# Kernel tuning notes

Hardware: AMD Instinct MI355X
Metric: run time of the kernel (lower is better)

## Reference

```python
import jax, jax.numpy as jnp
import numpy as np

N_NODES = 100000


def _sage_conv(x, edge_index, W_n, W_s, b):
    # edge_index: [2, E] with row0 = src, row1 = dst (messages flow src -> dst)
    src, dst = edge_index[0], edge_index[1]
    msgs = x[src]                                   # [E, F] gather
    summed = jax.ops.segment_sum(msgs, dst, num_segments=N_NODES)   # [N, F]
    deg = jax.ops.segment_sum(jnp.ones((edge_index.shape[1],), x.dtype), dst,
                              num_segments=N_NODES)                 # [N]
    mean = summed / jnp.maximum(deg, 1.0)[:, None]  # mean aggregation
    return mean @ W_n + x @ W_s + b


def setup_inputs() -> dict:
    key = jax.random.key(0)
    ks = jax.random.split(key, 8)
    in_dim, hid_dim, out_dim = 64, 64, 32
    n_edges = 1600000
    x = jax.random.normal(ks[0], (N_NODES, in_dim), dtype=jnp.float32)
    edge_index = jax.random.randint(ks[1], (2, n_edges), 0, N_NODES, dtype=jnp.int64)
    s1 = 1.0 / np.sqrt(in_dim)
    s2 = 1.0 / np.sqrt(hid_dim)
    W1_n = jax.random.uniform(ks[2], (in_dim, hid_dim), jnp.float32, -s1, s1)
    W1_s = jax.random.uniform(ks[3], (in_dim, hid_dim), jnp.float32, -s1, s1)
    b1 = jnp.zeros((hid_dim,), jnp.float32)
    W2_n = jax.random.uniform(ks[4], (hid_dim, out_dim), jnp.float32, -s2, s2)
    W2_s = jax.random.uniform(ks[5], (hid_dim, out_dim), jnp.float32, -s2, s2)
    b2 = jnp.zeros((out_dim,), jnp.float32)
    return {"x": x, "edge_index": edge_index, "W1_n": W1_n, "W1_s": W1_s,
            "b1": b1, "W2_n": W2_n, "W2_s": W2_s, "b2": b2}


def reference(x, edge_index, W1_n, W1_s, b1, W2_n, W2_s, b2):
    h = _sage_conv(x, edge_index, W1_n, W1_s, b1)
    h = jax.nn.relu(h)
    # dropout(p=0.5) is identity in eval mode
    out = _sage_conv(h, edge_index, W2_n, W2_s, b2)
    return out
```

## Files before the change

### kernel.cpp

```cpp
#include <hip/hip_runtime.h>
#include <hip/hip_bf16.h>

#define N_NODES 100000
#define NB 784
#define NPAD 100352
#define BSH 7
#define BMASK 127
#define CAP 4096
#define MSTRIDE 36

typedef float v2f __attribute__((ext_vector_type(2)));

__device__ inline void fma4(float a, const float4& w, float4& c) {
  c.x = fmaf(a, w.x, c.x);
  c.y = fmaf(a, w.y, c.y);
  c.z = fmaf(a, w.z, c.z);
  c.w = fmaf(a, w.w, c.w);
}
__device__ inline unsigned short f2bf(float f) {
  unsigned u = __float_as_uint(f);
  u += 0x7fffu + ((u >> 16) & 1u);
  return (unsigned short)(u >> 16);
}
__device__ inline unsigned pack2bf(float a, float b) {
  return (unsigned)f2bf(a) | ((unsigned)f2bf(b) << 16);
}
__device__ inline unsigned packfp8x4(float a, float b, float c, float d) {
  int pk = __builtin_amdgcn_cvt_pk_fp8_f32(a, b, 0, false);
  pk = __builtin_amdgcn_cvt_pk_fp8_f32(c, d, pk, true);
  return (unsigned)pk;
}
__device__ inline float4 relu_mix(uint2 m, uint2 s) {
  float4 v;
  v.x = fmaxf(__uint_as_float(m.x << 16) + __uint_as_float(s.x << 16), 0.f);
  v.y = fmaxf(__uint_as_float(m.x & 0xffff0000u) +
                  __uint_as_float(s.x & 0xffff0000u), 0.f);
  v.z = fmaxf(__uint_as_float(m.y << 16) + __uint_as_float(s.y << 16), 0.f);
  v.w = fmaxf(__uint_as_float(m.y & 0xffff0000u) +
                  __uint_as_float(s.y & 0xffff0000u), 0.f);
  return v;
}

#define EPB 8192
#define EPT 32
#define GB1 1563

__global__ __launch_bounds__(256) void fusedA_k(
    const int* __restrict__ src, const int* __restrict__ dst,
    unsigned* __restrict__ bcur, unsigned* __restrict__ ep,
    const float* __restrict__ x, const float* __restrict__ W1n,
    const float* __restrict__ W1s, const float* __restrict__ b1,
    unsigned* __restrict__ xnb8, unsigned short* __restrict__ xsb,
    int E, int NSB, int M) {
  __shared__ __align__(16) float smem[8192];
  const int tid = threadIdx.x;

  if ((int)blockIdx.x < NSB) {
    unsigned* lh = (unsigned*)smem;
    unsigned* lbase = lh + NB;
    for (int i = tid; i < NB; i += 256) lh[i] = 0;
    __syncthreads();
    const int ebase = blockIdx.x * EPB;
    unsigned rb[EPT];
#pragma unroll
    for (int it = 0; it < EPT; ++it) {
      int e = ebase + it * 256 + tid;
      if (e < E) {
        unsigned b = ((unsigned)dst[e]) >> BSH;
        unsigned r = atomicAdd(&lh[b], 1u);
        rb[it] = (r << 10) | b;
      }
    }
    __syncthreads();
    for (int i = tid; i < NB; i += 256)
      lbase[i] = lh[i] ? atomicAdd(&bcur[i], lh[i]) : 0u;
    __syncthreads();
#pragma unroll
    for (int it = 0; it < EPT; ++it) {
      int e = ebase + it * 256 + tid;
      if (e < E) {
        unsigned b = rb[it] & 1023u;
        unsigned r = rb[it] >> 10;
        ep[(size_t)b * CAP + lbase[b] + r] =
            (((unsigned)src[e]) << BSH) | (((unsigned)dst[e]) & BMASK);
      }
    }
    return;
  }

  float* Wn = smem;
  float* Ws = smem + 4096;
  const int row0 = ((int)blockIdx.x - NSB) * 64;

  for (int i = tid; i < 1024; i += 256) {
    ((float4*)Wn)[i] = ((const float4*)W1n)[i];
    ((float4*)Ws)[i] = ((const float4*)W1s)[i];
  }

  const int tx = tid & 15;
  const int ty = tid >> 4;
  const int arow = ty * 4;

  const float* xr[4];
#pragma unroll
  for (int r = 0; r < 4; ++r) {
    long long gr = row0 + arow + r;
    if (gr >= M) gr = M - 1;
    xr[r] = x + gr * 64;
  }

  float4 an[4], as[4];
#pragma unroll
  for (int r = 0; r < 4; ++r) {
    an[r] = make_float4(0.f, 0.f, 0.f, 0.f);
    as[r] = make_float4(0.f, 0.f, 0.f, 0.f);
  }
  __syncthreads();

#pragma unroll 2
  for (int k4 = 0; k4 < 16; ++k4) {
    float4 a[4];
#pragma unroll
    for (int r = 0; r < 4; ++r) a[r] = *(const float4*)(xr[r] + 4 * k4);
    float4 wn0 = *(const float4*)&Wn[(4 * k4 + 0) * 64 + 4 * tx];
    float4 wn1 = *(const float4*)&Wn[(4 * k4 + 1) * 64 + 4 * tx];
    float4 wn2 = *(const float4*)&Wn[(4 * k4 + 2) * 64 + 4 * tx];
    float4 wn3 = *(const float4*)&Wn[(4 * k4 + 3) * 64 + 4 * tx];
    float4 ws0 = *(const float4*)&Ws[(4 * k4 + 0) * 64 + 4 * tx];
    float4 ws1 = *(const float4*)&Ws[(4 * k4 + 1) * 64 + 4 * tx];
    float4 ws2 = *(const float4*)&Ws[(4 * k4 + 2) * 64 + 4 * tx];
    float4 ws3 = *(const float4*)&Ws[(4 * k4 + 3) * 64 + 4 * tx];
#pragma unroll
    for (int r = 0; r < 4; ++r) {
      fma4(a[r].x, wn0, an[r]);
      fma4(a[r].y, wn1, an[r]);
      fma4(a[r].z, wn2, an[r]);
      fma4(a[r].w, wn3, an[r]);
      fma4(a[r].x, ws0, as[r]);
      fma4(a[r].y, ws1, as[r]);
      fma4(a[r].z, ws2, as[r]);
      fma4(a[r].w, ws3, as[r]);
    }
  }

  const float4 bv = *(const float4*)&b1[4 * tx];
#pragma unroll
  for (int r = 0; r < 4; ++r) {
    int row = row0 + arow + r;
    if (row < M) {
      ushort4 ps;
      ps.x = f2bf(as[r].x + bv.x);
      ps.y = f2bf(as[r].y + bv.y);
      ps.z = f2bf(as[r].z + bv.z);
      ps.w = f2bf(as[r].w + bv.w);
      *(ushort4*)&xsb[(long long)row * 64 + 4 * tx] = ps;
      xnb8[(size_t)row * 16 + tx] =
          packfp8x4(an[r].x, an[r].y, an[r].z, an[r].w);
    }
  }
}

__global__ __launch_bounds__(256) void bsort_k(const unsigned* __restrict__ ep,
                                               const unsigned* __restrict__ bcur,
                                               int* __restrict__ ssrc,
                                               uint2* __restrict__ rows2) {
  __shared__ unsigned cnt[128];
  __shared__ unsigned sc[128];
  const int tid = threadIdx.x;
  const int b = blockIdx.x;
  const unsigned cntb = bcur[b];
  const unsigned beg = (unsigned)(b * CAP);
  if (tid < 128) cnt[tid] = 0;
  __syncthreads();
  for (unsigned j = tid; j < cntb; j += 256)
    atomicAdd(&cnt[ep[(size_t)beg + j] & BMASK], 1u);
  __syncthreads();
  unsigned v = (tid < 128) ? cnt[tid] : 0u;
  if (tid < 128) sc[tid] = v;
  __syncthreads();
  for (int off = 1; off < 128; off <<= 1) {
    unsigned t = (tid < 128 && tid >= off) ? sc[tid - off] : 0u;
    __syncthreads();
    if (tid < 128) sc[tid] += t;
    __syncthreads();
  }
  if (tid < 128) {
    unsigned ex = sc[tid] - v;
    rows2[b * 128 + tid] = make_uint2(beg + ex, beg + ex + v);
    cnt[tid] = ex;
  }
  __syncthreads();
  for (unsigned j = tid; j < cntb; j += 256) {
    unsigned p = ep[(size_t)beg + j];
    unsigned r = atomicAdd(&cnt[p & BMASK], 1u);
    ssrc[(size_t)beg + r] = (int)(p >> BSH);
  }
}

__global__ __launch_bounds__(256) void fgg_k(
    const uint4* __restrict__ valb4, const int* __restrict__ ssrc,
    const uint2* __restrict__ rows2, const unsigned short* __restrict__ xsb,
    const float* __restrict__ W2n, const float* __restrict__ W2s,
    const float* __restrict__ b2, unsigned* __restrict__ hnb8,
    float* __restrict__ hs, int M) {
  __shared__ float Wn[64 * 32];
  __shared__ float Ws[64 * 32];
  __shared__ unsigned mlds[64 * MSTRIDE];
  const int tid = threadIdx.x;
  const int node0 = blockIdx.x * 64;

  for (int i = tid; i < 512; i += 256) {
    ((float4*)Wn)[i] = ((const float4*)W2n)[i];
    ((float4*)Ws)[i] = ((const float4*)W2s)[i];
  }

  constexpr int P = 4;
  const int lrow = tid / P;
  const int node = node0 + lrow;
  const int p = tid & 3;
  const uint2 be = rows2[node];
  const unsigned beg = be.x, end = be.y;

  float acc[16];
#pragma unroll
  for (int q = 0; q < 16; ++q) acc[q] = 0.f;

  unsigned j = beg;
  for (; j + 8 <= end; j += 8) {
    int sn[8];
#pragma unroll
    for (int i = 0; i < 8; ++i) sn[i] = ssrc[j + i];
    uint4 u[8];
#pragma unroll
    for (int i = 0; i < 8; ++i) u[i] = valb4[(size_t)sn[i] * P + p];
#pragma unroll
    for (int i = 0; i < 8; ++i) {
      v2f f0 = __builtin_amdgcn_cvt_pk_f32_fp8((int)u[i].x, false);
      v2f f1 = __builtin_amdgcn_cvt_pk_f32_fp8((int)u[i].x, true);
      v2f f2 = __builtin_amdgcn_cvt_pk_f32_fp8((int)u[i].y, false);
      v2f f3 = __builtin_amdgcn_cvt_pk_f32_fp8((int)u[i].y, true);
      v2f f4 = __builtin_amdgcn_cvt_pk_f32_fp8((int)u[i].z, false);
      v2f f5 = __builtin_amdgcn_cvt_pk_f32_fp8((int)u[i].z, true);
      v2f f6 = __builtin_amdgcn_cvt_pk_f32_fp8((int)u[i].w, false);
      v2f f7 = __builtin_amdgcn_cvt_pk_f32_fp8((int)u[i].w, true);
      acc[0] += f0[0];  acc[1] += f0[1];
      acc[2] += f1[0];  acc[3] += f1[1];
      acc[4] += f2[0];  acc[5] += f2[1];
      acc[6] += f3[0];  acc[7] += f3[1];
      acc[8] += f4[0];  acc[9] += f4[1];
      acc[10] += f5[0]; acc[11] += f5[1];
      acc[12] += f6[0]; acc[13] += f6[1];
      acc[14] += f7[0]; acc[15] += f7[1];
    }
  }
  if (j < end) {
    const unsigned last = end - 1;
    int sn[8];
#pragma unroll
    for (int i = 0; i < 8; ++i) {
      unsigned jj = j + i;
      sn[i] = ssrc[jj < last ? jj : last];
    }
    uint4 u[8];
#pragma unroll
    for (int i = 0; i < 8; ++i) u[i] = valb4[(size_t)sn[i] * P + p];
#pragma unroll
    for (int i = 0; i < 8; ++i) {
      float w = ((j + i) < end) ? 1.f : 0.f;
      v2f f0 = __builtin_amdgcn_cvt_pk_f32_fp8((int)u[i].x, false);
      v2f f1 = __builtin_amdgcn_cvt_pk_f32_fp8((int)u[i].x, true);
      v2f f2 = __builtin_amdgcn_cvt_pk_f32_fp8((int)u[i].y, false);
      v2f f3 = __builtin_amdgcn_cvt_pk_f32_fp8((int)u[i].y, true);
      v2f f4 = __builtin_amdgcn_cvt_pk_f32_fp8((int)u[i].z, false);
      v2f f5 = __builtin_amdgcn_cvt_pk_f32_fp8((int)u[i].z, true);
      v2f f6 = __builtin_amdgcn_cvt_pk_f32_fp8((int)u[i].w, false);
      v2f f7 = __builtin_amdgcn_cvt_pk_f32_fp8((int)u[i].w, true);
      acc[0] = fmaf(w, f0[0], acc[0]);   acc[1] = fmaf(w, f0[1], acc[1]);
      acc[2] = fmaf(w, f1[0], acc[2]);   acc[3] = fmaf(w, f1[1], acc[3]);
      acc[4] = fmaf(w, f2[0], acc[4]);   acc[5] = fmaf(w, f2[1], acc[5]);
      acc[6] = fmaf(w, f3[0], acc[6]);   acc[7] = fmaf(w, f3[1], acc[7]);
      acc[8] = fmaf(w, f4[0], acc[8]);   acc[9] = fmaf(w, f4[1], acc[9]);
      acc[10] = fmaf(w, f5[0], acc[10]); acc[11] = fmaf(w, f5[1], acc[11]);
      acc[12] = fmaf(w, f6[0], acc[12]); acc[13] = fmaf(w, f6[1], acc[13]);
      acc[14] = fmaf(w, f7[0], acc[14]); acc[15] = fmaf(w, f7[1], acc[15]);
    }
  }

  const unsigned dg = end - beg;
  const float inv = dg ? 1.f / (float)dg : 0.f;
  uint4 pk0, pk1;
  pk0.x = pack2bf(acc[0] * inv, acc[1] * inv);
  pk0.y = pack2bf(acc[2] * inv, acc[3] * inv);
  pk0.z = pack2bf(acc[4] * inv, acc[5] * inv);
  pk0.w = pack2bf(acc[6] * inv, acc[7] * inv);
  pk1.x = pack2bf(acc[8] * inv, acc[9] * inv);
  pk1.y = pack2bf(acc[10] * inv, acc[11] * inv);
  pk1.z = pack2bf(acc[12] * inv, acc[13] * inv);
  pk1.w = pack2bf(acc[14] * inv, acc[15] * inv);
  *(uint4*)&mlds[lrow * MSTRIDE + p * 8] = pk0;
  *(uint4*)&mlds[lrow * MSTRIDE + p * 8 + 4] = pk1;
  __syncthreads();

  const int tx = tid & 7;
  const int ty = tid >> 3;
  const int arow = ty * 2;

  const uint2* mp[2];
  const uint2* sp[2];
#pragma unroll
  for (int r = 0; r < 2; ++r) {
    long long gr = node0 + arow + r;
    if (gr >= M) gr = M - 1;
    mp[r] = (const uint2*)&mlds[(arow + r) * MSTRIDE];
    sp[r] = (const uint2*)(xsb + gr * 64);
  }

  float4 an[2], as[2];
#pragma unroll
  for (int r = 0; r < 2; ++r) {
    an[r] = make_float4(0.f, 0.f, 0.f, 0.f);
    as[r] = make_float4(0.f, 0.f, 0.f, 0.f);
  }

#pragma unroll 2
  for (int k4 = 0; k4 < 16; ++k4) {
    float4 a[2];
#pragma unroll
    for (int r = 0; r < 2; ++r) a[r] = relu_mix(mp[r][k4], sp[r][k4]);
    float4 wn0 = *(const float4*)&Wn[(4 * k4 + 0) * 32 + 4 * tx];
    float4 wn1 = *(const float4*)&Wn[(4 * k4 + 1) * 32 + 4 * tx];
    float4 wn2 = *(const float4*)&Wn[(4 * k4 + 2) * 32 + 4 * tx];
    float4 wn3 = *(const float4*)&Wn[(4 * k4 + 3) * 32 + 4 * tx];
    float4 ws0 = *(const float4*)&Ws[(4 * k4 + 0) * 32 + 4 * tx];
    float4 ws1 = *(const float4*)&Ws[(4 * k4 + 1) * 32 + 4 * tx];
    float4 ws2 = *(const float4*)&Ws[(4 * k4 + 2) * 32 + 4 * tx];
    float4 ws3 = *(const float4*)&Ws[(4 * k4 + 3) * 32 + 4 * tx];
#pragma unroll
    for (int r = 0; r < 2; ++r) {
      fma4(a[r].x, wn0, an[r]);
      fma4(a[r].y, wn1, an[r]);
      fma4(a[r].z, wn2, an[r]);
      fma4(a[r].w, wn3, an[r]);
      fma4(a[r].x, ws0, as[r]);
      fma4(a[r].y, ws1, as[r]);
      fma4(a[r].z, ws2, as[r]);
      fma4(a[r].w, ws3, as[r]);
    }
  }

  const float4 bv = *(const float4*)&b2[4 * tx];
#pragma unroll
  for (int r = 0; r < 2; ++r) {
    int row = node0 + arow + r;
    if (row < M) {
      float4 o;
      o.x = as[r].x + bv.x;
      o.y = as[r].y + bv.y;
      o.z = as[r].z + bv.z;
      o.w = as[r].w + bv.w;
      *(float4*)&hs[(long long)row * 32 + 4 * tx] = o;
      hnb8[(size_t)row * 8 + tx] =
          packfp8x4(an[r].x, an[r].y, an[r].z, an[r].w);
    }
  }
}

__global__ __launch_bounds__(256) void gather2_k(
    const uint4* __restrict__ valb4, const int* __restrict__ ssrc,
    const uint2* __restrict__ rows2, const float* __restrict__ base,
    float* __restrict__ out, int N) {
  constexpr int P = 2;
  const int node = blockIdx.x * 128 + threadIdx.x / P;
  const int p = threadIdx.x & 1;
  if (node >= N) return;
  const uint2 be = rows2[node];
  const unsigned beg = be.x, end = be.y;

  float acc[16];
#pragma unroll
  for (int q = 0; q < 16; ++q) acc[q] = 0.f;

  unsigned j = beg;
  for (; j + 8 <= end; j += 8) {
    int sn[8];
#pragma unroll
    for (int i = 0; i < 8; ++i) sn[i] = ssrc[j + i];
    uint4 u[8];
#pragma unroll
    for (int i = 0; i < 8; ++i) u[i] = valb4[(size_t)sn[i] * P + p];
#pragma unroll
    for (int i = 0; i < 8; ++i) {
      v2f f0 = __builtin_amdgcn_cvt_pk_f32_fp8((int)u[i].x, false);
      v2f f1 = __builtin_amdgcn_cvt_pk_f32_fp8((int)u[i].x, true);
      v2f f2 = __builtin_amdgcn_cvt_pk_f32_fp8((int)u[i].y, false);
      v2f f3 = __builtin_amdgcn_cvt_pk_f32_fp8((int)u[i].y, true);
      v2f f4 = __builtin_amdgcn_cvt_pk_f32_fp8((int)u[i].z, false);
      v2f f5 = __builtin_amdgcn_cvt_pk_f32_fp8((int)u[i].z, true);
      v2f f6 = __builtin_amdgcn_cvt_pk_f32_fp8((int)u[i].w, false);
      v2f f7 = __builtin_amdgcn_cvt_pk_f32_fp8((int)u[i].w, true);
      acc[0] += f0[0];  acc[1] += f0[1];
      acc[2] += f1[0];  acc[3] += f1[1];
      acc[4] += f2[0];  acc[5] += f2[1];
      acc[6] += f3[0];  acc[7] += f3[1];
      acc[8] += f4[0];  acc[9] += f4[1];
      acc[10] += f5[0]; acc[11] += f5[1];
      acc[12] += f6[0]; acc[13] += f6[1];
      acc[14] += f7[0]; acc[15] += f7[1];
    }
  }
  if (j < end) {
    const unsigned last = end - 1;
    int sn[8];
#pragma unroll
    for (int i = 0; i < 8; ++i) {
      unsigned jj = j + i;
      sn[i] = ssrc[jj < last ? jj : last];
    }
    uint4 u[8];
#pragma unroll
    for (int i = 0; i < 8; ++i) u[i] = valb4[(size_t)sn[i] * P + p];
#pragma unroll
    for (int i = 0; i < 8; ++i) {
      float w = ((j + i) < end) ? 1.f : 0.f;
      v2f f0 = __builtin_amdgcn_cvt_pk_f32_fp8((int)u[i].x, false);
      v2f f1 = __builtin_amdgcn_cvt_pk_f32_fp8((int)u[i].x, true);
      v2f f2 = __builtin_amdgcn_cvt_pk_f32_fp8((int)u[i].y, false);
      v2f f3 = __builtin_amdgcn_cvt_pk_f32_fp8((int)u[i].y, true);
      v2f f4 = __builtin_amdgcn_cvt_pk_f32_fp8((int)u[i].z, false);
      v2f f5 = __builtin_amdgcn_cvt_pk_f32_fp8((int)u[i].z, true);
      v2f f6 = __builtin_amdgcn_cvt_pk_f32_fp8((int)u[i].w, false);
      v2f f7 = __builtin_amdgcn_cvt_pk_f32_fp8((int)u[i].w, true);
      acc[0] = fmaf(w, f0[0], acc[0]);   acc[1] = fmaf(w, f0[1], acc[1]);
      acc[2] = fmaf(w, f1[0], acc[2]);   acc[3] = fmaf(w, f1[1], acc[3]);
      acc[4] = fmaf(w, f2[0], acc[4]);   acc[5] = fmaf(w, f2[1], acc[5]);
      acc[6] = fmaf(w, f3[0], acc[6]);   acc[7] = fmaf(w, f3[1], acc[7]);
      acc[8] = fmaf(w, f4[0], acc[8]);   acc[9] = fmaf(w, f4[1], acc[9]);
      acc[10] = fmaf(w, f5[0], acc[10]); acc[11] = fmaf(w, f5[1], acc[11]);
      acc[12] = fmaf(w, f6[0], acc[12]); acc[13] = fmaf(w, f6[1], acc[13]);
      acc[14] = fmaf(w, f7[0], acc[14]); acc[15] = fmaf(w, f7[1], acc[15]);
    }
  }

  const unsigned dg = end - beg;
  const float inv = dg ? 1.f / (float)dg : 0.f;
  const size_t o = (size_t)node * 32 + 16 * p;
#pragma unroll
  for (int q4 = 0; q4 < 4; ++q4) {
    float4 bv = *(const float4*)&base[o + 4 * q4];
    float4 ov;
    ov.x = acc[4 * q4 + 0] * inv + bv.x;
    ov.y = acc[4 * q4 + 1] * inv + bv.y;
    ov.z = acc[4 * q4 + 2] * inv + bv.z;
    ov.w = acc[4 * q4 + 3] * inv + bv.w;
    *(float4*)&out[o + 4 * q4] = ov;
  }
}

extern "C" void kernel_launch(void* const* d_in, const int* in_sizes, int n_in,
                              void* d_out, int out_size, void* d_ws,
                              size_t ws_size, hipStream_t stream) {
  const float* x   = (const float*)d_in[0];
  const int*   ei  = (const int*)d_in[1];
  const float* W1n = (const float*)d_in[2];
  const float* W1s = (const float*)d_in[3];
  const float* b1  = (const float*)d_in[4];
  const float* W2n = (const float*)d_in[5];
  const float* W2s = (const float*)d_in[6];
  const float* b2  = (const float*)d_in[7];
  float* out = (float*)d_out;

  const int E = in_sizes[1] / 2;
  const int M = N_NODES;
  const int* src = ei;
  const int* dst = ei + E;
  const int NSB = (E + EPB - 1) / EPB;

  char* wsb = (char*)d_ws;
  unsigned*       ep    = (unsigned*)(wsb);
  int*            ssrc  = (int*)(wsb + 12845056);
  uint2*          rows2 = (uint2*)(wsb + 25690112);
  unsigned*       bcur  = (unsigned*)(wsb + 26492928);
  unsigned*       xnb8  = (unsigned*)(wsb + 26496064);
  unsigned short* xsb   = (unsigned short*)(wsb + 32896064);
  float*          hs    = (float*)(wsb + 45696064);
  unsigned*       hnb8  = (unsigned*)(wsb);

  hipMemsetAsync(bcur, 0, NB * 4, stream);
  fusedA_k<<<NSB + GB1, 256, 0, stream>>>(src, dst, bcur, ep, x, W1n, W1s, b1,
                                          xnb8, xsb, E, NSB, M);
  bsort_k<<<NB, 256, 0, stream>>>(ep, bcur, ssrc, rows2);
  fgg_k<<<GB1, 256, 0, stream>>>((const uint4*)xnb8, ssrc, rows2, xsb, W2n,
                                 W2s, b2, hnb8, hs, M);
  gather2_k<<<(M + 127) / 128, 256, 0, stream>>>((const uint4*)hnb8, ssrc,
                                                 rows2, hs, out, M);
}
```

Measured before the change: 195.9 us.

## Merge edge binning into GEMM blocks using direct global atomics

Removes the separate edge-binning blocks. Every layer-1 GEMM block now also bins 1024 edges: it loads src/dst, then claims a slot in its destination bucket with one global atomicAdd per edge before starting the GEMM. This drops the shared-memory histogram, its barriers and the extra blocks, and lets edge loads overlap the weight staging. The cost is about 1.6M global atomics on only 784 counters instead of one atomic per bucket per block, which risks heavy contention.

Result: slower. 543.4 us (+177.4%).

```diff
diff --git a/kernel.cpp b/kernel.cpp
--- a/kernel.cpp
+++ b/kernel.cpp
@@ -41,62 +41,51 @@
   return v;
 }
 
-#define EPB 8192
-#define EPT 32
 #define GB1 1563
-
-__global__ __launch_bounds__(256) void fusedA_k(
+#define SEPB 1024
+
+__global__ __launch_bounds__(256) void fusedB_k(
     const int* __restrict__ src, const int* __restrict__ dst,
     unsigned* __restrict__ bcur, unsigned* __restrict__ ep,
     const float* __restrict__ x, const float* __restrict__ W1n,
     const float* __restrict__ W1s, const float* __restrict__ b1,
     unsigned* __restrict__ xnb8, unsigned short* __restrict__ xsb,
-    int E, int NSB, int M) {
+    int E, int M) {
   __shared__ __align__(16) float smem[8192];
-  const int tid = threadIdx.x;
-
-  if ((int)blockIdx.x < NSB) {
-    unsigned* lh = (unsigned*)smem;
-    unsigned* lbase = lh + NB;
-    for (int i = tid; i < NB; i += 256) lh[i] = 0;
-    __syncthreads();
-    const int ebase = blockIdx.x * EPB;
-    unsigned rb[EPT];
-#pragma unroll
-    for (int it = 0; it < EPT; ++it) {
-      int e = ebase + it * 256 + tid;
-      if (e < E) {
-        unsigned b = ((unsigned)dst[e]) >> BSH;
-        unsigned r = atomicAdd(&lh[b], 1u);
-        rb[it] = (r << 10) | b;
-      }
-    }
-    __syncthreads();
-    for (int i = tid; i < NB; i += 256)
-      lbase[i] = lh[i] ? atomicAdd(&bcur[i], lh[i]) : 0u;
-    __syncthreads();
-#pragma unroll
-    for (int it = 0; it < EPT; ++it) {
-      int e = ebase + it * 256 + tid;
-      if (e < E) {
-        unsigned b = rb[it] & 1023u;
-        unsigned r = rb[it] >> 10;
-        ep[(size_t)b * CAP + lbase[b] + r] =
-            (((unsigned)src[e]) << BSH) | (((unsigned)dst[e]) & BMASK);
-      }
-    }
-    return;
-  }
-
   float* Wn = smem;
   float* Ws = smem + 4096;
-  const int row0 = ((int)blockIdx.x - NSB) * 64;
+  const int tid = threadIdx.x;
+  const int bid = blockIdx.x;
+
+  const int ebase = bid * SEPB;
+  int es[4], ed[4];
+  bool ev[4];
+#pragma unroll
+  for (int it = 0; it < 4; ++it) {
+    int e = ebase + it * 256 + tid;
+    ev[it] = (e < E);
+    if (ev[it]) {
+      es[it] = src[e];
+      ed[it] = dst[e];
+    }
+  }
 
   for (int i = tid; i < 1024; i += 256) {
     ((float4*)Wn)[i] = ((const float4*)W1n)[i];
     ((float4*)Ws)[i] = ((const float4*)W1s)[i];
   }
 
+#pragma unroll
+  for (int it = 0; it < 4; ++it) {
+    if (ev[it]) {
+      unsigned b = ((unsigned)ed[it]) >> BSH;
+      unsigned r = atomicAdd(&bcur[b], 1u);
+      ep[(size_t)b * CAP + r] =
+          (((unsigned)es[it]) << BSH) | (((unsigned)ed[it]) & BMASK);
+    }
+  }
+
+  const int row0 = bid * 64;
   const int tx = tid & 15;
   const int ty = tid >> 4;
   const int arow = ty * 4;
@@ -473,7 +462,6 @@
   const int M = N_NODES;
   const int* src = ei;
   const int* dst = ei + E;
-  const int NSB = (E + EPB - 1) / EPB;
 
   char* wsb = (char*)d_ws;
   unsigned*       ep    = (unsigned*)(wsb);
@@ -486,8 +474,8 @@
   unsigned*       hnb8  = (unsigned*)(wsb);
 
   hipMemsetAsync(bcur, 0, NB * 4, stream);
-  fusedA_k<<<NSB + GB1, 256, 0, stream>>>(src, dst, bcur, ep, x, W1n, W1s, b1,
-                                          xnb8, xsb, E, NSB, M);
+  fusedB_k<<<GB1, 256, 0, stream>>>(src, dst, bcur, ep, x, W1n, W1s, b1,
+                                    xnb8, xsb, E, M);
   bsort_k<<<NB, 256, 0, stream>>>(ep, bcur, ssrc, rows2);
   fgg_k<<<GB1, 256, 0, stream>>>((const uint4*)xnb8, ssrc, rows2, xsb, W2n,
                                  W2s, b2, hnb8, hs, M);
```

## Sort nodes by degree within each block to balance gather work per wavefront

Applied to the files above, without the earlier changes.

Both gather kernels now load per-node degrees into shared memory, rank the nodes in the block by degree, and assign threads to nodes in sorted order. Nodes with similar degree then share a wavefront, which is meant to reduce divergence and idle lanes in the edge loop. The tail handling also changes from clamped-index loads with weight masking to predicated loads that zero unused slots. The cost is an extra rows2 read, an O(64) or O(128) ranking loop per node, and two additional barriers. Reads of rows2 past N in the last block rely on padding.

New measurement: 216.1 us. 1.1x slower.

```diff
diff --git a/kernel.cpp b/kernel.cpp
--- a/kernel.cpp
+++ b/kernel.cpp
@@ -39,6 +39,24 @@
   v.w = fmaxf(__uint_as_float(m.y & 0xffff0000u) +
                   __uint_as_float(s.y & 0xffff0000u), 0.f);
   return v;
+}
+__device__ inline void acc16(const uint4& u, float* acc) {
+  v2f f0 = __builtin_amdgcn_cvt_pk_f32_fp8((int)u.x, false);
+  v2f f1 = __builtin_amdgcn_cvt_pk_f32_fp8((int)u.x, true);
+  v2f f2 = __builtin_amdgcn_cvt_pk_f32_fp8((int)u.y, false);
+  v2f f3 = __builtin_amdgcn_cvt_pk_f32_fp8((int)u.y, true);
+  v2f f4 = __builtin_amdgcn_cvt_pk_f32_fp8((int)u.z, false);
+  v2f f5 = __builtin_amdgcn_cvt_pk_f32_fp8((int)u.z, true);
+  v2f f6 = __builtin_amdgcn_cvt_pk_f32_fp8((int)u.w, false);
+  v2f f7 = __builtin_amdgcn_cvt_pk_f32_fp8((int)u.w, true);
+  acc[0] += f0[0];  acc[1] += f0[1];
+  acc[2] += f1[0];  acc[3] += f1[1];
+  acc[4] += f2[0];  acc[5] += f2[1];
+  acc[6] += f3[0];  acc[7] += f3[1];
+  acc[8] += f4[0];  acc[9] += f4[1];
+  acc[10] += f5[0]; acc[11] += f5[1];
+  acc[12] += f6[0]; acc[13] += f6[1];
+  acc[14] += f7[0]; acc[15] += f7[1];
 }
 
 #define EPB 8192
@@ -206,6 +224,9 @@
   __shared__ float Wn[64 * 32];
   __shared__ float Ws[64 * 32];
   __shared__ unsigned mlds[64 * MSTRIDE];
+  __shared__ unsigned degs[64];
+  __shared__ unsigned begs[64];
+  __shared__ unsigned char perm[64];
   const int tid = threadIdx.x;
   const int node0 = blockIdx.x * 64;
 
@@ -214,12 +235,29 @@
     ((float4*)Ws)[i] = ((const float4*)W2s)[i];
   }
 
-  constexpr int P = 4;
-  const int lrow = tid / P;
-  const int node = node0 + lrow;
+  if (tid < 64) {
+    uint2 be = rows2[node0 + tid];
+    degs[tid] = be.y - be.x;
+    begs[tid] = be.x;
+  }
+  __syncthreads();
+  if (tid < 64) {
+    unsigned d = degs[tid];
+    int rank = 0;
+    for (int j2 = 0; j2 < 64; ++j2) {
+      unsigned dj = degs[j2];
+      rank += (dj < d) || (dj == d && j2 < tid);
+    }
+    perm[rank] = (unsigned char)tid;
+  }
+  __syncthreads();
+
+  const int slot = tid >> 2;
+  const int lrow = perm[slot];
   const int p = tid & 3;
-  const uint2 be = rows2[node];
-  const unsigned beg = be.x, end = be.y;
+  const unsigned dg = degs[lrow];
+  const unsigned beg = begs[lrow];
+  const unsigned end = beg + dg;
 
   float acc[16];
 #pragma unroll
@@ -232,61 +270,24 @@
     for (int i = 0; i < 8; ++i) sn[i] = ssrc[j + i];
     uint4 u[8];
 #pragma unroll
-    for (int i = 0; i < 8; ++i) u[i] = valb4[(size_t)sn[i] * P + p];
+    for (int i = 0; i < 8; ++i) u[i] = valb4[(size_t)sn[i] * 4 + p];
+#pragma unroll
+    for (int i = 0; i < 8; ++i) acc16(u[i], acc);
+  }
+  if (j < end) {
+    uint4 u[8];
 #pragma unroll
     for (int i = 0; i < 8; ++i) {
-      v2f f0 = __builtin_amdgcn_cvt_pk_f32_fp8((int)u[i].x, false);
-      v2f f1 = __builtin_amdgcn_cvt_pk_f32_fp8((int)u[i].x, true);
-      v2f f2 = __builtin_amdgcn_cvt_pk_f32_fp8((int)u[i].y, false);
-      v2f f3 = __builtin_amdgcn_cvt_pk_f32_fp8((int)u[i].y, true);
-      v2f f4 = __builtin_amdgcn_cvt_pk_f32_fp8((int)u[i].z, false);
-      v2f f5 = __builtin_amdgcn_cvt_pk_f32_fp8((int)u[i].z, true);
-      v2f f6 = __builtin_amdgcn_cvt_pk_f32_fp8((int)u[i].w, false);
-      v2f f7 = __builtin_amdgcn_cvt_pk_f32_fp8((int)u[i].w, true);
-      acc[0] += f0[0];  acc[1] += f0[1];
-      acc[2] += f1[0];  acc[3] += f1[1];
-      acc[4] += f2[0];  acc[5] += f2[1];
-      acc[6] += f3[0];  acc[7] += f3[1];
-      acc[8] += f4[0];  acc[9] += f4[1];
-      acc[10] += f5[0]; acc[11] += f5[1];
-      acc[12] += f6[0]; acc[13] += f6[1];
-      acc[14] += f7[0]; acc[15] += f7[1];
-    }
-  }
-  if (j < end) {
-    const unsigned last = end - 1;
-    int sn[8];
-#pragma unroll
-    for (int i = 0; i < 8; ++i) {
-      unsigned jj = j + i;
-      sn[i] = ssrc[jj < last ? jj : last];
-    }
-    uint4 u[8];
-#pragma unroll
-    for (int i = 0; i < 8; ++i) u[i] = valb4[(size_t)sn[i] * P + p];
-#pragma unroll
-    for (int i = 0; i < 8; ++i) {
-      float w = ((j + i) < end) ? 1.f : 0.f;
-      v2f f0 = __builtin_amdgcn_cvt_pk_f32_fp8((int)u[i].x, false);
-      v2f f1 = __builtin_amdgcn_cvt_pk_f32_fp8((int)u[i].x, true);
-      v2f f2 = __builtin_amdgcn_cvt_pk_f32_fp8((int)u[i].y, false);
-      v2f f3 = __builtin_amdgcn_cvt_pk_f32_fp8((int)u[i].y, true);
-      v2f f4 = __builtin_amdgcn_cvt_pk_f32_fp8((int)u[i].z, false);
-      v2f f5 = __builtin_amdgcn_cvt_pk_f32_fp8((int)u[i].z, true);
-      v2f f6 = __builtin_amdgcn_cvt_pk_f32_fp8((int)u[i].w, false);
-      v2f f7 = __builtin_amdgcn_cvt_pk_f32_fp8((int)u[i].w, true);
-      acc[0] = fmaf(w, f0[0], acc[0]);   acc[1] = fmaf(w, f0[1], acc[1]);
-      acc[2] = fmaf(w, f1[0], acc[2]);   acc[3] = fmaf(w, f1[1], acc[3]);
-      acc[4] = fmaf(w, f2[0], acc[4]);   acc[5] = fmaf(w, f2[1], acc[5]);
-      acc[6] = fmaf(w, f3[0], acc[6]);   acc[7] = fmaf(w, f3[1], acc[7]);
-      acc[8] = fmaf(w, f4[0], acc[8]);   acc[9] = fmaf(w, f4[1], acc[9]);
-      acc[10] = fmaf(w, f5[0], acc[10]); acc[11] = fmaf(w, f5[1], acc[11]);
-      acc[12] = fmaf(w, f6[0], acc[12]); acc[13] = fmaf(w, f6[1], acc[13]);
-      acc[14] = fmaf(w, f7[0], acc[14]); acc[15] = fmaf(w, f7[1], acc[15]);
-    }
-  }
-
-  const unsigned dg = end - beg;
+      u[i] = make_uint4(0u, 0u, 0u, 0u);
+      if (j + i < end) {
+        int s = ssrc[j + i];
+        u[i] = valb4[(size_t)s * 4 + p];
+      }
+    }
+#pragma unroll
+    for (int i = 0; i < 8; ++i) acc16(u[i], acc);
+  }
+
   const float inv = dg ? 1.f / (float)dg : 0.f;
   uint4 pk0, pk1;
   pk0.x = pack2bf(acc[0] * inv, acc[1] * inv);
@@ -369,12 +370,36 @@
     const uint4* __restrict__ valb4, const int* __restrict__ ssrc,
     const uint2* __restrict__ rows2, const float* __restrict__ base,
     float* __restrict__ out, int N) {
-  constexpr int P = 2;
-  const int node = blockIdx.x * 128 + threadIdx.x / P;
-  const int p = threadIdx.x & 1;
-  if (node >= N) return;
-  const uint2 be = rows2[node];
-  const unsigned beg = be.x, end = be.y;
+  __shared__ unsigned degs[128];
+  __shared__ unsigned begs[128];
+  __shared__ unsigned char perm[128];
+  const int tid = threadIdx.x;
+  const int node0 = blockIdx.x * 128;
+
+  if (tid < 128) {
+    uint2 be = rows2[node0 + tid];
+    degs[tid] = be.y - be.x;
+    begs[tid] = be.x;
+  }
+  __syncthreads();
+  if (tid < 128) {
+    unsigned d = degs[tid];
+    int rank = 0;
+    for (int j2 = 0; j2 < 128; ++j2) {
+      unsigned dj = degs[j2];
+      rank += (dj < d) || (dj == d && j2 < tid);
+    }
+    perm[rank] = (unsigned char)tid;
+  }
+  __syncthreads();
+
+  const int slot = tid >> 1;
+  const int lrow = perm[slot];
+  const int node = node0 + lrow;
+  const int p = tid & 1;
+  const unsigned dg = degs[lrow];
+  const unsigned beg = begs[lrow];
+  const unsigned end = beg + dg;
 
   float acc[16];
 #pragma unroll
@@ -387,72 +412,37 @@
     for (int i = 0; i < 8; ++i) sn[i] = ssrc[j + i];
     uint4 u[8];
 #pragma unroll
-    for (int i = 0; i < 8; ++i) u[i] = valb4[(size_t)sn[i] * P + p];
+    for (int i = 0; i < 8; ++i) u[i] = valb4[(size_t)sn[i] * 2 + p];
+#pragma unroll
+    for (int i = 0; i < 8; ++i) acc16(u[i], acc);
+  }
+  if (j < end) {
+    uint4 u[8];
 #pragma unroll
     for (int i = 0; i < 8; ++i) {
-      v2f f0 = __builtin_amdgcn_cvt_pk_f32_fp8((int)u[i].x, false);
-      v2f f1 = __builtin_amdgcn_cvt_pk_f32_fp8((int)u[i].x, true);
-      v2f f2 = __builtin_amdgcn_cvt_pk_f32_fp8((int)u[i].y, false);
-      v2f f3 = __builtin_amdgcn_cvt_pk_f32_fp8((int)u[i].y, true);
-      v2f f4 = __builtin_amdgcn_cvt_pk_f32_fp8((int)u[i].z, false);
-      v2f f5 = __builtin_amdgcn_cvt_pk_f32_fp8((int)u[i].z, true);
-      v2f f6 = __builtin_amdgcn_cvt_pk_f32_fp8((int)u[i].w, false);
-      v2f f7 = __builtin_amdgcn_cvt_pk_f32_fp8((int)u[i].w, true);
-      acc[0] += f0[0];  acc[1] += f0[1];
-      acc[2] += f1[0];  acc[3] += f1[1];
-      acc[4] += f2[0];  acc[5] += f2[1];
-      acc[6] += f3[0];  acc[7] += f3[1];
-      acc[8] += f4[0];  acc[9] += f4[1];
-      acc[10] += f5[0]; acc[11] += f5[1];
-      acc[12] += f6[0]; acc[13] += f6[1];
-      acc[14] += f7[0]; acc[15] += f7[1];
-    }
-  }
-  if (j < end) {
-    const unsigned last = end - 1;
-    int sn[8];
-#pragma unroll
-    for (int i = 0; i < 8; ++i) {
-      unsigned jj = j + i;
-      sn[i] = ssrc[jj < last ? jj : last];
-    }
-    uint4 u[8];
-#pragma unroll
-    for (int i = 0; i < 8; ++i) u[i] = valb4[(size_t)sn[i] * P + p];
-#pragma unroll
-    for (int i = 0; i < 8; ++i) {
-      float w = ((j + i) < end) ? 1.f : 0.f;
-      v2f f0 = __builtin_amdgcn_cvt_pk_f32_fp8((int)u[i].x, false);
-      v2f f1 = __builtin_amdgcn_cvt_pk_f32_fp8((int)u[i].x, true);
-      v2f f2 = __builtin_amdgcn_cvt_pk_f32_fp8((int)u[i].y, false);
-      v2f f3 = __builtin_amdgcn_cvt_pk_f32_fp8((int)u[i].y, true);
-      v2f f4 = __builtin_amdgcn_cvt_pk_f32_fp8((int)u[i].z, false);
-      v2f f5 = __builtin_amdgcn_cvt_pk_f32_fp8((int)u[i].z, true);
-      v2f f6 = __builtin_amdgcn_cvt_pk_f32_fp8((int)u[i].w, false);
-      v2f f7 = __builtin_amdgcn_cvt_pk_f32_fp8((int)u[i].w, true);
-      acc[0] = fmaf(w, f0[0], acc[0]);   acc[1] = fmaf(w, f0[1], acc[1]);
-      acc[2] = fmaf(w, f1[0], acc[2]);   acc[3] = fmaf(w, f1[1], acc[3]);
-      acc[4] = fmaf(w, f2[0], acc[4]);   acc[5] = fmaf(w, f2[1], acc[5]);
-      acc[6] = fmaf(w, f3[0], acc[6]);   acc[7] = fmaf(w, f3[1], acc[7]);
-      acc[8] = fmaf(w, f4[0], acc[8]);   acc[9] = fmaf(w, f4[1], acc[9]);
-      acc[10] = fmaf(w, f5[0], acc[10]); acc[11] = fmaf(w, f5[1], acc[11]);
-      acc[12] = fmaf(w, f6[0], acc[12]); acc[13] = fmaf(w, f6[1], acc[13]);
-      acc[14] = fmaf(w, f7[0], acc[14]); acc[15] = fmaf(w, f7[1], acc[15]);
-    }
-  }
-
-  const unsigned dg = end - beg;
-  const float inv = dg ? 1.f / (float)dg : 0.f;
-  const size_t o = (size_t)node * 32 + 16 * p;
-#pragma unroll
-  for (int q4 = 0; q4 < 4; ++q4) {
-    float4 bv = *(const float4*)&base[o + 4 * q4];
-    float4 ov;
-    ov.x = acc[4 * q4 + 0] * inv + bv.x;
-    ov.y = acc[4 * q4 + 1] * inv + bv.y;
-    ov.z = acc[4 * q4 + 2] * inv + bv.z;
-    ov.w = acc[4 * q4 + 3] * inv + bv.w;
-    *(float4*)&out[o + 4 * q4] = ov;
+      u[i] = make_uint4(0u, 0u, 0u, 0u);
+      if (j + i < end) {
+        int s = ssrc[j + i];
+        u[i] = valb4[(size_t)s * 2 + p];
+      }
+    }
+#pragma unroll
+    for (int i = 0; i < 8; ++i) acc16(u[i], acc);
+  }
+
+  if (node < N) {
+    const float inv = dg ? 1.f / (float)dg : 0.f;
+    const size_t o = (size_t)node * 32 + 16 * p;
+#pragma unroll
+    for (int q4 = 0; q4 < 4; ++q4) {
+      float4 bv = *(const float4*)&base[o + 4 * q4];
+      float4 ov;
+      ov.x = acc[4 * q4 + 0] * inv + bv.x;
+      ov.y = acc[4 * q4 + 1] * inv + bv.y;
+      ov.z = acc[4 * q4 + 2] * inv + bv.z;
+      ov.w = acc[4 * q4 + 3] * inv + bv.w;
+      *(float4*)&out[o + 4 * q4] = ov;
+    }
   }
 }
 
```
